# Kernel optimization log

Measured on AMD Instinct MI355X. Metric: run time of the kernel, lower is better.

## Reference

```python
import jax, jax.numpy as jnp
import numpy as np

B, T, DIM, H, DH = 4, 2048, 1024, 16, 64
NEG = -1.0e9


def setup_inputs() -> dict:
    key = jax.random.key(0)
    ks = jax.random.split(key, 12)
    inner = H * DH
    s_in = 1.0 / np.sqrt(DIM)
    s_out = 1.0 / np.sqrt(inner)
    q = jax.random.normal(ks[0], (B, T, DIM), jnp.float32)
    k = jax.random.normal(ks[1], (B, T, DIM), jnp.float32)
    v = jax.random.normal(ks[2], (B, T, DIM), jnp.float32)
    # nn.Linear weights stored as [out, in]; we keep [in, out] for x @ W
    W_q = jax.random.uniform(ks[3], (DIM, inner), jnp.float32, -s_in, s_in)
    b_q = jax.random.uniform(ks[4], (inner,), jnp.float32, -s_in, s_in)
    W_k = jax.random.uniform(ks[5], (DIM, inner), jnp.float32, -s_in, s_in)
    b_k = jax.random.uniform(ks[6], (inner,), jnp.float32, -s_in, s_in)
    W_v = jax.random.uniform(ks[7], (DIM, inner), jnp.float32, -s_in, s_in)
    b_v = jax.random.uniform(ks[8], (inner,), jnp.float32, -s_in, s_in)
    W_o = jax.random.uniform(ks[9], (inner, DIM), jnp.float32, -s_out, s_out)
    b_o = jax.random.uniform(ks[10], (DIM,), jnp.float32, -s_out, s_out)
    # causal mask: True = masked (strict upper triangle), broadcastable [1,1,T,T]
    causal_mask = jnp.triu(jnp.ones((T, T), bool), k=1)[None, None]
    # context mask: True = keep; random padding pattern with col 0 always valid
    context_mask = jax.random.bernoulli(ks[11], 0.9, (B, T)).at[:, 0].set(True)
    return {"q": q, "k": k, "v": v,
            "W_q": W_q, "b_q": b_q, "W_k": W_k, "b_k": b_k,
            "W_v": W_v, "b_v": b_v, "W_o": W_o, "b_o": b_o,
            "causal_mask": causal_mask, "context_mask": context_mask}


def reference(q, k, v, W_q, b_q, W_k, b_k, W_v, b_v, W_o, b_o,
              causal_mask, context_mask):
    scale = DH ** -0.5
    split = lambda x: x.reshape(x.shape[0], x.shape[1], H, DH).transpose(0, 2, 1, 3)
    qh = split(q @ W_q + b_q)  # [b,h,t,d]
    kh = split(k @ W_k + b_k)
    vh = split(v @ W_v + b_v)
    scores = jnp.einsum('bhid,bhjd->bhij', qh * scale, kh)
    scores = jnp.where(context_mask[:, None, None, :], scores, NEG)
    scores = jnp.where(causal_mask, NEG, scores)
    probs = jax.nn.softmax(scores, axis=-1)
    out = jnp.einsum('bhij,bhjd->bhid', probs, vh)
    out = out.transpose(0, 2, 1, 3).reshape(B, T, H * DH)
    return out @ W_o + b_o
```

## Files before the change

kernel.cpp:

```cpp
#include <hip/hip_runtime.h>
#include <hip/hip_bf16.h>
#include <cstdint>
#include <cstddef>

#define DEV static __device__ __forceinline__

typedef __attribute__((ext_vector_type(8))) short short8;
typedef __attribute__((ext_vector_type(4))) float floatx4;

#define BB 4
#define TT 2048
#define DIMM 1024
#define HH 16
#define DHH 64
#define MM (BB*TT)
#define QBLK 128
#define NQT (TT/QBLK)
#define M0F 12.0f

DEV unsigned short f2bu(float f) {
    unsigned int u = __float_as_uint(f);
    unsigned int r = (u + 0x7fffu + ((u >> 16) & 1u)) >> 16;
    return (unsigned short)r;
}

DEV unsigned long long pack4(float a, float b, float c, float d) {
    return (unsigned long long)f2bu(a) | ((unsigned long long)f2bu(b) << 16) |
           ((unsigned long long)f2bu(c) << 32) | ((unsigned long long)f2bu(d) << 48);
}

DEV unsigned int pk2(float lo, float hi) {
    __hip_bfloat162 h = __float22bfloat162_rn(make_float2(lo, hi));
    unsigned int r;
    __builtin_memcpy(&r, &h, 4);
    return r;
}

DEV unsigned long long pk4(float a, float b, float c, float d) {
    return (unsigned long long)pk2(a, b) | ((unsigned long long)pk2(c, d) << 32);
}

DEV void gload16(const void* g, void* l) {
    __builtin_amdgcn_global_load_lds(
        (const __attribute__((address_space(1))) unsigned int*)g,
        (__attribute__((address_space(3))) unsigned int*)l, 16, 0, 0);
}

#define MFMA16(a, b, c) __builtin_amdgcn_mfma_f32_16x16x32_bf16((a), (b), (c), 0, 0, 0)

__global__ __launch_bounds__(256) void ctx_bias(const unsigned char* __restrict__ raw,
                                                float* __restrict__ out) {
    __shared__ int nz1, nz23;
    if (threadIdx.x == 0) { nz1 = 0; nz23 = 0; }
    __syncthreads();
    int a1 = 0, a23 = 0;
    for (int i = threadIdx.x; i < BB * TT; i += 256) {
        unsigned char vb = raw[i];
        int m = i & 3;
        if (vb) { if (m == 1) a1 = 1; else if (m >= 2) a23 = 1; }
    }
    if (a1) atomicOr(&nz1, 1);
    if (a23) atomicOr(&nz23, 1);
    __syncthreads();
    const int mode = nz1 ? 2 : (nz23 ? 1 : 0);
    for (int i = threadIdx.x; i < BB * TT; i += 256) {
        bool keep;
        if (mode == 2)      keep = raw[i] != 0;
        else if (mode == 0) keep = raw[(size_t)4 * i] != 0;
        else                keep = (raw[(size_t)4 * i + 2] | raw[(size_t)4 * i + 3]) != 0;
        out[i] = keep ? -M0F : -3.0e38f;
    }
}

__global__ __launch_bounds__(256) void wtrans(const float* __restrict__ W0, const float* __restrict__ W1,
                                              const float* __restrict__ W2, const float* __restrict__ W3,
                                              unsigned short* __restrict__ out) {
    const float* W = blockIdx.y == 0 ? W0 : blockIdx.y == 1 ? W1 : blockIdx.y == 2 ? W2 : W3;
    unsigned short* O = out + (size_t)blockIdx.y * DIMM * DIMM;
    const int tx = blockIdx.x & 15, ty = blockIdx.x >> 4;
    __shared__ float s[64][65];
    const int tid = threadIdx.x;
#pragma unroll
    for (int j = 0; j < 4; ++j) {
        int c = tid + 256 * j;
        int r = c >> 4, c4 = c & 15;
        float4 vv = *reinterpret_cast<const float4*>(&W[(size_t)(ty * 64 + r) * DIMM + tx * 64 + c4 * 4]);
        s[r][c4 * 4 + 0] = vv.x; s[r][c4 * 4 + 1] = vv.y;
        s[r][c4 * 4 + 2] = vv.z; s[r][c4 * 4 + 3] = vv.w;
    }
    __syncthreads();
#pragma unroll
    for (int j = 0; j < 4; ++j) {
        int c = tid + 256 * j;
        int n = c >> 4, k4 = c & 15;
        unsigned long long pk = pack4(s[k4 * 4 + 0][n], s[k4 * 4 + 1][n], s[k4 * 4 + 2][n], s[k4 * 4 + 3][n]);
        *reinterpret_cast<unsigned long long*>(&O[(size_t)(tx * 64 + n) * DIMM + ty * 64 + k4 * 4]) = pk;
    }
}

__global__ __launch_bounds__(256) void cvt_bf16(const float* __restrict__ in,
                                                unsigned short* __restrict__ out) {
    const size_t i = ((size_t)blockIdx.x * 256 + threadIdx.x) * 8;
    float4 a = *reinterpret_cast<const float4*>(&in[i]);
    float4 b = *reinterpret_cast<const float4*>(&in[i + 4]);
    unsigned long long lo = pk4(a.x, a.y, a.z, a.w);
    unsigned long long hi = pk4(b.x, b.y, b.z, b.w);
    ulonglong2 v; v.x = lo; v.y = hi;
    *reinterpret_cast<ulonglong2*>(&out[i]) = v;
}

template <int OMODE>
__global__ __launch_bounds__(256) void gemm_bf16(const unsigned short* __restrict__ Ab,
                                                 const unsigned short* __restrict__ Bt,
                                                 const float* __restrict__ bias,
                                                 void* __restrict__ Cp, float scale) {
    __shared__ unsigned short As[128 * 64];
    __shared__ unsigned short Bs[128 * 64];
    const int tid = threadIdx.x, lane = tid & 63, g = lane >> 4, lq = lane & 15;
    const int wid = tid >> 6;
    const int mbase = blockIdx.x * 128, nbase = blockIdx.y * 128;
    const int wm = (wid >> 1) * 64, wn = (wid & 1) * 64;
    floatx4 acc[4][4];
#pragma unroll
    for (int i = 0; i < 4; ++i)
#pragma unroll
        for (int j = 0; j < 4; ++j) acc[i][j] = (floatx4){0.f, 0.f, 0.f, 0.f};

    for (int k0 = 0; k0 < DIMM; k0 += 64) {
#pragma unroll
        for (int j = 0; j < 4; ++j) {
            const int c = j * 256 + tid;
            const int row = c >> 3, ci = c & 7;
            const int sc = ci ^ (row & 7);
            gload16(&Ab[(size_t)(mbase + row) * DIMM + k0 + sc * 8], &As[c * 8]);
            gload16(&Bt[(size_t)(nbase + row) * DIMM + k0 + sc * 8], &Bs[c * 8]);
        }
        __syncthreads();
#pragma unroll
        for (int kk = 0; kk < 2; ++kk) {
            short8 af[4], bf[4];
#pragma unroll
            for (int i = 0; i < 4; ++i) {
                const int ra = wm + i * 16 + lq;
                af[i] = *reinterpret_cast<const short8*>(&As[ra * 64 + ((kk * 4 + g) ^ (ra & 7)) * 8]);
                const int rb = wn + i * 16 + lq;
                bf[i] = *reinterpret_cast<const short8*>(&Bs[rb * 64 + ((kk * 4 + g) ^ (rb & 7)) * 8]);
            }
#pragma unroll
            for (int i = 0; i < 4; ++i)
#pragma unroll
                for (int j2 = 0; j2 < 4; ++j2)
                    acc[i][j2] = MFMA16(af[i], bf[j2], acc[i][j2]);
        }
        __syncthreads();
    }

#pragma unroll
    for (int i = 0; i < 4; ++i) {
#pragma unroll
        for (int j = 0; j < 4; ++j) {
            const int col = nbase + wn + j * 16 + lq;
            const float bvv = bias[col];
            const int row0 = mbase + wm + i * 16 + g * 4;
            if (OMODE == 2) {
                float* C = (float*)Cp;
#pragma unroll
                for (int r = 0; r < 4; ++r)
                    C[(size_t)(row0 + r) * DIMM + col] = acc[i][j][r] + bvv;
            } else if (OMODE == 0) {
                unsigned short* C = (unsigned short*)Cp;
#pragma unroll
                for (int r = 0; r < 4; ++r)
                    C[(size_t)(row0 + r) * DIMM + col] = f2bu((acc[i][j][r] + bvv) * scale);
            } else {
                unsigned short* C = (unsigned short*)Cp;
                const int b = row0 >> 11, t0 = row0 & (TT - 1);
                const int h = col >> 6, d = col & 63;
                unsigned long long pk = pk4(acc[i][j][0] + bvv, acc[i][j][1] + bvv,
                                            acc[i][j][2] + bvv, acc[i][j][3] + bvv);
                *reinterpret_cast<unsigned long long*>(
                    &C[((size_t)(b * HH + h) * DHH + d) * TT + t0]) = pk;
            }
        }
    }
}

__global__ __launch_bounds__(512, 4) void attn128(const unsigned short* __restrict__ Q,
                                                  const unsigned short* __restrict__ Km,
                                                  const unsigned short* __restrict__ Vt,
                                                  const float* __restrict__ ctxb,
                                                  unsigned short* __restrict__ O) {
    const int pair = blockIdx.x & 7, h = (blockIdx.x >> 3) & 15, b = blockIdx.x >> 7;
    const int tid = threadIdx.x, lane = tid & 63, g = lane >> 4, lq = lane & 15, wid = tid >> 6;

    __shared__ unsigned short Qs[QBLK * 64];
    __shared__ unsigned short Ks[2][64 * 64];
    __shared__ unsigned short Vs[2][64 * 64];
    __shared__ unsigned short Ps[8][16 * 72];

    const float* cbias = ctxb + b * TT;
    const unsigned short* Vbase = Vt + (size_t)(b * HH + h) * DHH * TT;
    const int srow = tid >> 3, sdc = tid & 7;
    const int soff = (srow * 128 + sdc * 16) ^ ((srow & 7) << 4);

    for (int part = 0; part < 2; ++part) {
        const int qt = (part == 0) ? pair : (NQT - 1 - pair);
        const int qbase = qt * QBLK;
        const size_t rowQ = (size_t)(b * TT + qbase);
        const int nkv = 2 * qt + 2;

        __syncthreads();
#pragma unroll
        for (int j = 0; j < 2; ++j) {
            int ci = j * 512 + tid;
            int row = ci >> 3, dc = ci & 7;
            *reinterpret_cast<float4*>((char*)Qs + ((row * 128 + dc * 16) ^ ((row & 7) << 4))) =
                *reinterpret_cast<const float4*>(&Q[(rowQ + row) * DIMM + h * DHH + dc * 8]);
        }
        {
            float4 k0v = *reinterpret_cast<const float4*>(&Km[(size_t)(b * TT + srow) * DIMM + h * DHH + sdc * 8]);
            float4 v0v = *reinterpret_cast<const float4*>(&Vbase[(size_t)srow * TT + sdc * 8]);
            *reinterpret_cast<float4*>((char*)Ks[0] + soff) = k0v;
            *reinterpret_cast<float4*>((char*)Vs[0] + soff) = v0v;
        }
        __syncthreads();

        short8 qf0, qf1;
        {
            const int r = wid * 16 + lq;
            const int sw = (r & 7) << 4;
            qf0 = *reinterpret_cast<const short8*>((char*)Qs + ((r * 128 + g * 16) ^ sw));
            qf1 = *reinterpret_cast<const short8*>((char*)Qs + ((r * 128 + 64 + g * 16) ^ sw));
        }

        floatx4 oacc[4];
#pragma unroll
        for (int f = 0; f < 4; ++f) oacc[f] = (floatx4){0.f, 0.f, 0.f, 0.f};
        float l_run = 0.f;
        const int qwave_min = qbase + wid * 16;
        const int qg = qwave_min + lq;

        for (int kt = 0; kt < nkv; ++kt) {
            const int cur = kt & 1;
            const int kvb = kt * 64;
            const bool pf = (kt + 1 < nkv);
            float4 kreg, vreg;
            if (pf) {
                const int kvn = kvb + 64;
                kreg = *reinterpret_cast<const float4*>(&Km[(size_t)(b * TT + kvn + srow) * DIMM + h * DHH + sdc * 8]);
                vreg = *reinterpret_cast<const float4*>(&Vbase[(size_t)srow * TT + kvn + sdc * 8]);
            }
            if (kvb <= qwave_min + 15) {
                const bool needC = (kvb + 63 > qwave_min);
                float p[4][4];
                __builtin_amdgcn_s_setprio(1);
#pragma unroll
                for (int f = 0; f < 4; ++f) {
                    const int r = f * 16 + lq;
                    const int sw = (r & 7) << 4;
                    short8 kf0 = *reinterpret_cast<const short8*>((char*)Ks[cur] + ((r * 128 + g * 16) ^ sw));
                    short8 kf1 = *reinterpret_cast<const short8*>((char*)Ks[cur] + ((r * 128 + 64 + g * 16) ^ sw));
                    const float4 bias = *reinterpret_cast<const float4*>(&cbias[kvb + f * 16 + g * 4]);
                    floatx4 t = (floatx4){bias.x, bias.y, bias.z, bias.w};
                    t = MFMA16(kf0, qf0, t);
                    t = MFMA16(kf1, qf1, t);
#pragma unroll
                    for (int r2 = 0; r2 < 4; ++r2) {
                        float sv = t[r2];
                        if (needC) {
                            const int kv = kvb + f * 16 + g * 4 + r2;
                            if (kv > qg) sv = -3.0e38f;
                        }
                        p[f][r2] = exp2f(sv);
                    }
                }
                __builtin_amdgcn_s_setprio(0);
                float rs = 0.f;
#pragma unroll
                for (int f = 0; f < 4; ++f)
#pragma unroll
                    for (int r2 = 0; r2 < 4; ++r2) rs += p[f][r2];
                rs += __shfl_xor(rs, 16, 64);
                rs += __shfl_xor(rs, 32, 64);
                l_run += rs;
#pragma unroll
                for (int f = 0; f < 4; ++f)
                    *reinterpret_cast<unsigned long long*>(&Ps[wid][lq * 72 + f * 16 + g * 4]) =
                        pk4(p[f][0], p[f][1], p[f][2], p[f][3]);
                __builtin_amdgcn_s_setprio(1);
#pragma unroll
                for (int f = 0; f < 4; ++f) {
                    const int r = f * 16 + lq;
                    const int sw = (r & 7) << 4;
#pragma unroll
                    for (int kk = 0; kk < 2; ++kk) {
                        short8 av = *reinterpret_cast<const short8*>((char*)Vs[cur] + ((r * 128 + kk * 64 + g * 16) ^ sw));
                        short8 bv = *reinterpret_cast<const short8*>(&Ps[wid][lq * 72 + kk * 32 + g * 8]);
                        oacc[f] = MFMA16(av, bv, oacc[f]);
                    }
                }
                __builtin_amdgcn_s_setprio(0);
            }
            if (pf) {
                *reinterpret_cast<float4*>((char*)Ks[cur ^ 1] + soff) = kreg;
                *reinterpret_cast<float4*>((char*)Vs[cur ^ 1] + soff) = vreg;
            }
            __syncthreads();
        }

        const float inv = 1.f / l_run;
#pragma unroll
        for (int f = 0; f < 4; ++f) {
            unsigned long long pk = pk4(oacc[f][0] * inv, oacc[f][1] * inv,
                                        oacc[f][2] * inv, oacc[f][3] * inv);
            *reinterpret_cast<unsigned long long*>(
                &O[(rowQ + wid * 16 + lq) * DIMM + h * DHH + f * 16 + g * 4]) = pk;
        }
    }
}

extern "C" void kernel_launch(void* const* d_in, const int* in_sizes, int n_in,
                              void* d_out, int out_size, void* d_ws, size_t ws_size,
                              hipStream_t stream) {
    const float* q  = (const float*)d_in[0];
    const float* k  = (const float*)d_in[1];
    const float* v  = (const float*)d_in[2];
    const float* Wq = (const float*)d_in[3];
    const float* bq = (const float*)d_in[4];
    const float* Wk = (const float*)d_in[5];
    const float* bk = (const float*)d_in[6];
    const float* Wv = (const float*)d_in[7];
    const float* bv = (const float*)d_in[8];
    const float* Wo = (const float*)d_in[9];
    const float* bo = (const float*)d_in[10];
    const unsigned char* cmask = (const unsigned char*)d_in[12];

    unsigned short* Qp  = (unsigned short*)d_ws;
    unsigned short* Kp  = Qp + (size_t)MM * DIMM;
    unsigned short* Vtp = Kp + (size_t)MM * DIMM;
    unsigned short* AO  = Vtp + (size_t)MM * DIMM;
    unsigned short* Wt  = AO + (size_t)MM * DIMM;
    float* ctxb = (float*)(Wt + (size_t)4 * DIMM * DIMM);

    ctx_bias<<<dim3(1), dim3(256), 0, stream>>>(cmask, ctxb);
    wtrans<<<dim3(256, 4), dim3(256), 0, stream>>>(Wq, Wk, Wv, Wo, Wt);

    const float scale_q = 0.125f * 1.4426950408889634f;

    cvt_bf16<<<dim3(4096), dim3(256), 0, stream>>>(q, AO);
    gemm_bf16<0><<<dim3(64, 8), dim3(256), 0, stream>>>(AO, Wt,                           bq, Qp,  scale_q);
    cvt_bf16<<<dim3(4096), dim3(256), 0, stream>>>(k, AO);
    gemm_bf16<0><<<dim3(64, 8), dim3(256), 0, stream>>>(AO, Wt + (size_t)DIMM * DIMM,     bk, Kp,  1.f);
    cvt_bf16<<<dim3(4096), dim3(256), 0, stream>>>(v, AO);
    gemm_bf16<1><<<dim3(64, 8), dim3(256), 0, stream>>>(AO, Wt + (size_t)2 * DIMM * DIMM, bv, Vtp, 1.f);

    attn128<<<dim3(BB * HH * 8), dim3(512), 0, stream>>>(Qp, Kp, Vtp, ctxb, AO);

    gemm_bf16<2><<<dim3(64, 8), dim3(256), 0, stream>>>(AO, Wt + (size_t)3 * DIMM * DIMM, bo, d_out, 1.f);
}
```

Before: 234.7 us.

## Double-buffer GEMM loads, keep P in registers for PV MFMA, remap attention blocks

After: 224.2 us. 1.05x faster.

```diff
diff --git a/kernel.cpp b/kernel.cpp
--- a/kernel.cpp
+++ b/kernel.cpp
@@ -6,6 +6,7 @@
 #define DEV static __device__ __forceinline__
 
 typedef __attribute__((ext_vector_type(8))) short short8;
+typedef __attribute__((ext_vector_type(4))) short short4v;
 typedef __attribute__((ext_vector_type(4))) float floatx4;
 
 #define BB 4
@@ -47,6 +48,21 @@
 }
 
 #define MFMA16(a, b, c) __builtin_amdgcn_mfma_f32_16x16x32_bf16((a), (b), (c), 0, 0, 0)
+
+#if defined(__has_builtin)
+#if __has_builtin(__builtin_amdgcn_mfma_f32_16x16x16bf16_1k)
+#define HAVE_MFMA_K16 1
+#endif
+#endif
+
+DEV floatx4 mfma_k16(short4v a, short4v b, floatx4 c) {
+#ifdef HAVE_MFMA_K16
+    return __builtin_amdgcn_mfma_f32_16x16x16bf16_1k(a, b, c, 0, 0, 0);
+#else
+    asm volatile("v_mfma_f32_16x16x16_bf16 %0, %1, %2, %0" : "+v"(c) : "v"(a), "v"(b));
+    return c;
+#endif
+}
 
 __global__ __launch_bounds__(256) void ctx_bias(const unsigned char* __restrict__ raw,
                                                 float* __restrict__ out) {
@@ -114,8 +130,8 @@
                                                  const unsigned short* __restrict__ Bt,
                                                  const float* __restrict__ bias,
                                                  void* __restrict__ Cp, float scale) {
-    __shared__ unsigned short As[128 * 64];
-    __shared__ unsigned short Bs[128 * 64];
+    __shared__ unsigned short As[2][128 * 64];
+    __shared__ unsigned short Bs[2][128 * 64];
     const int tid = threadIdx.x, lane = tid & 63, g = lane >> 4, lq = lane & 15;
     const int wid = tid >> 6;
     const int mbase = blockIdx.x * 128, nbase = blockIdx.y * 128;
@@ -126,25 +142,33 @@
 #pragma unroll
         for (int j = 0; j < 4; ++j) acc[i][j] = (floatx4){0.f, 0.f, 0.f, 0.f};
 
+#define STAGE(buf, k0)                                                              \
+    {                                                                               \
+        _Pragma("unroll")                                                           \
+        for (int j = 0; j < 4; ++j) {                                               \
+            const int c = j * 256 + tid;                                            \
+            const int row = c >> 3, ci = c & 7;                                     \
+            const int sc = ci ^ (row & 7);                                          \
+            gload16(&Ab[(size_t)(mbase + row) * DIMM + (k0) + sc * 8], &As[buf][c * 8]); \
+            gload16(&Bt[(size_t)(nbase + row) * DIMM + (k0) + sc * 8], &Bs[buf][c * 8]); \
+        }                                                                           \
+    }
+
+    STAGE(0, 0);
+    asm volatile("s_waitcnt vmcnt(0)");
+    __syncthreads();
+    int cur = 0;
     for (int k0 = 0; k0 < DIMM; k0 += 64) {
-#pragma unroll
-        for (int j = 0; j < 4; ++j) {
-            const int c = j * 256 + tid;
-            const int row = c >> 3, ci = c & 7;
-            const int sc = ci ^ (row & 7);
-            gload16(&Ab[(size_t)(mbase + row) * DIMM + k0 + sc * 8], &As[c * 8]);
-            gload16(&Bt[(size_t)(nbase + row) * DIMM + k0 + sc * 8], &Bs[c * 8]);
-        }
-        __syncthreads();
+        if (k0 + 64 < DIMM) STAGE(cur ^ 1, k0 + 64);
 #pragma unroll
         for (int kk = 0; kk < 2; ++kk) {
             short8 af[4], bf[4];
 #pragma unroll
             for (int i = 0; i < 4; ++i) {
                 const int ra = wm + i * 16 + lq;
-                af[i] = *reinterpret_cast<const short8*>(&As[ra * 64 + ((kk * 4 + g) ^ (ra & 7)) * 8]);
+                af[i] = *reinterpret_cast<const short8*>(&As[cur][ra * 64 + ((kk * 4 + g) ^ (ra & 7)) * 8]);
                 const int rb = wn + i * 16 + lq;
-                bf[i] = *reinterpret_cast<const short8*>(&Bs[rb * 64 + ((kk * 4 + g) ^ (rb & 7)) * 8]);
+                bf[i] = *reinterpret_cast<const short8*>(&Bs[cur][rb * 64 + ((kk * 4 + g) ^ (rb & 7)) * 8]);
             }
 #pragma unroll
             for (int i = 0; i < 4; ++i)
@@ -153,7 +177,9 @@
                     acc[i][j2] = MFMA16(af[i], bf[j2], acc[i][j2]);
         }
         __syncthreads();
-    }
+        cur ^= 1;
+    }
+#undef STAGE
 
 #pragma unroll
     for (int i = 0; i < 4; ++i) {
@@ -190,13 +216,12 @@
                                                   const unsigned short* __restrict__ Vt,
                                                   const float* __restrict__ ctxb,
                                                   unsigned short* __restrict__ O) {
-    const int pair = blockIdx.x & 7, h = (blockIdx.x >> 3) & 15, b = blockIdx.x >> 7;
+    const int pair = blockIdx.x >> 6, h = blockIdx.x & 15, b = (blockIdx.x >> 4) & 3;
     const int tid = threadIdx.x, lane = tid & 63, g = lane >> 4, lq = lane & 15, wid = tid >> 6;
 
     __shared__ unsigned short Qs[QBLK * 64];
     __shared__ unsigned short Ks[2][64 * 64];
     __shared__ unsigned short Vs[2][64 * 64];
-    __shared__ unsigned short Ps[8][16 * 72];
 
     const float* cbias = ctxb + b * TT;
     const unsigned short* Vbase = Vt + (size_t)(b * HH + h) * DHH * TT;
@@ -283,23 +308,29 @@
                 rs += __shfl_xor(rs, 16, 64);
                 rs += __shfl_xor(rs, 32, 64);
                 l_run += rs;
-#pragma unroll
-                for (int f = 0; f < 4; ++f)
-                    *reinterpret_cast<unsigned long long*>(&Ps[wid][lq * 72 + f * 16 + g * 4]) =
-                        pk4(p[f][0], p[f][1], p[f][2], p[f][3]);
+                short4v w[4];
+#pragma unroll
+                for (int f = 0; f < 4; ++f) {
+                    unsigned long long pw = pk4(p[f][0], p[f][1], p[f][2], p[f][3]);
+                    __builtin_memcpy(&w[f], &pw, 8);
+                }
                 __builtin_amdgcn_s_setprio(1);
 #pragma unroll
                 for (int f = 0; f < 4; ++f) {
                     const int r = f * 16 + lq;
                     const int sw = (r & 7) << 4;
-#pragma unroll
-                    for (int kk = 0; kk < 2; ++kk) {
-                        short8 av = *reinterpret_cast<const short8*>((char*)Vs[cur] + ((r * 128 + kk * 64 + g * 16) ^ sw));
-                        short8 bv = *reinterpret_cast<const short8*>(&Ps[wid][lq * 72 + kk * 32 + g * 8]);
-                        oacc[f] = MFMA16(av, bv, oacc[f]);
+                    const int rb = r * 128;
+#pragma unroll
+                    for (int j = 0; j < 4; ++j) {
+                        short4v av = *reinterpret_cast<const short4v*>(
+                            (char*)Vs[cur] + ((rb + j * 32 + g * 8) ^ sw));
+                        oacc[f] = mfma_k16(av, w[j], oacc[f]);
                     }
                 }
                 __builtin_amdgcn_s_setprio(0);
+#ifndef HAVE_MFMA_K16
+                asm volatile("s_nop 7\ns_nop 7");
+#endif
             }
             if (pf) {
                 *reinterpret_cast<float4*>((char*)Ks[cur ^ 1] + soff) = kreg;
```
